# Kernel tuning notes

Measured on AMD Instinct MI355X. Metric: run time of the kernel, lower is better.

## Reference

```python
import jax, jax.numpy as jnp
import numpy as np

N = 60000   # cells
F = 256     # CELL_FEATURE_DIM
H = 128     # HIDDEN_DIM
NH = 8      # NUM_HEADS
DH = H // NH
L = 2       # NUM_LAYERS
C = 256     # tissue clusters
E = 600000  # cell edges
ET = 1500   # tissue edges
NCLS = 4


def _seg_softmax(s, seg, n):
    # numerically stable softmax within segments; s: [E, NH]
    m = jax.ops.segment_max(s, seg, num_segments=n)
    e = jnp.exp(s - m[seg])
    z = jax.ops.segment_sum(e, seg, num_segments=n)
    return e / z[seg]


def _forward(cell_features, cluster_labels, cell_edge_index, tissue_edge_index,
             W_cell_proj, b_cell_proj, W_tissue_proj, b_tissue_proj,
             gat_W, gat_asrc, gat_adst, gat_b, gcn_W, gcn_b,
             bu_Wq, bu_Wk, bu_Wv, bu_bq, bu_bk, bu_bv, bu_Wo, bu_bo,
             td_Wv, td_bv, td_Wo, td_bo,
             gru_Wih, gru_bih, gru_Whh, gru_bhh,
             Wc1, bc1, Wc2, bc2, Wc3, bc3):
    lab = cluster_labels
    # tissue node init = per-cluster mean of raw cell features (as in _construct_tissue_graph)
    cnt = jax.ops.segment_sum(jnp.ones((N,), jnp.float32), lab, num_segments=C)
    tissue_x = jax.ops.segment_sum(cell_features, lab, num_segments=C) / jnp.maximum(cnt, 1.0)[:, None]

    cell_h = cell_features @ W_cell_proj.T + b_cell_proj      # [N, H]
    tissue_h = tissue_x @ W_tissue_proj.T + b_tissue_proj     # [C, H]

    # add self-loops (PyG GATConv / GCNConv default)
    csrc = jnp.concatenate([cell_edge_index[0], jnp.arange(N, dtype=cell_edge_index.dtype)])
    cdst = jnp.concatenate([cell_edge_index[1], jnp.arange(N, dtype=cell_edge_index.dtype)])
    tsrc = jnp.concatenate([tissue_edge_index[0], jnp.arange(C, dtype=tissue_edge_index.dtype)])
    tdst = jnp.concatenate([tissue_edge_index[1], jnp.arange(C, dtype=tissue_edge_index.dtype)])

    # GCN symmetric norm (deg over col, PyG gcn_norm)
    degc = jax.ops.segment_sum(jnp.ones_like(tdst, dtype=jnp.float32), tdst, num_segments=C)
    dinv = jnp.where(degc > 0, 1.0 / jnp.sqrt(degc), 0.0)
    w_e = (dinv[tsrc] * dinv[tdst])[:, None]

    scale = 1.0 / jnp.sqrt(jnp.float32(DH))

    for l in range(L):
        # --- GATConv (multi-head concat) + ELU ---
        h = (cell_h @ gat_W[l].T).reshape(N, NH, DH)
        a_s = (h * gat_asrc[l]).sum(-1)  # [N, NH]
        a_d = (h * gat_adst[l]).sum(-1)
        e = jax.nn.leaky_relu(a_s[csrc] + a_d[cdst], negative_slope=0.2)  # [E+N, NH]
        alpha = _seg_softmax(e, cdst, N)
        agg = jax.ops.segment_sum(h[csrc] * alpha[:, :, None], cdst, num_segments=N)
        cell_h = jax.nn.elu(agg.reshape(N, H) + gat_b[l])

        # --- GCNConv + ReLU on tissue graph ---
        th = tissue_h @ gcn_W[l].T
        tissue_h = jax.nn.relu(jax.ops.segment_sum(th[tsrc] * w_e, tdst, num_segments=C) + gcn_b[l])

        # --- bottom-up cross-level attention: tissue queries attend over their cells ---
        q = ((tissue_h @ bu_Wq.T + bu_bq) * scale).reshape(C, NH, DH)
        k = (cell_h @ bu_Wk.T + bu_bk).reshape(N, NH, DH)
        v = (cell_h @ bu_Wv.T + bu_bv).reshape(N, NH, DH)
        s_att = (q[lab] * k).sum(-1)                       # [N, NH]
        al = _seg_softmax(s_att, lab, C)
        ctx = jax.ops.segment_sum(v * al[:, :, None], lab, num_segments=C).reshape(C, H)
        tissue_h = ctx @ bu_Wo.T + bu_bo

        # --- top-down attention: each cell attends to its single tissue node ---
        # softmax over one key is identically 1, so output = Wo(Wv t + bv) + bo gathered per cell
        td = (tissue_h @ td_Wv.T + td_bv) @ td_Wo.T + td_bo  # [C, H]
        cell_h = td[lab]

        # --- top-down GRUCell refinement: x=[cell;tissue], h=cell ---
        x_in = jnp.concatenate([cell_h, tissue_h[lab]], axis=-1)  # [N, 2H]
        gi = x_in @ gru_Wih.T + gru_bih
        gh = cell_h @ gru_Whh.T + gru_bhh
        r = jax.nn.sigmoid(gi[:, :H] + gh[:, :H])
        z = jax.nn.sigmoid(gi[:, H:2 * H] + gh[:, H:2 * H])
        n = jnp.tanh(gi[:, 2 * H:] + r * gh[:, 2 * H:])
        cell_h = (1.0 - z) * n + z * cell_h

    # dual-pooling readouts (single graph: batch all zeros)
    emb = jnp.concatenate([cell_h.mean(0), cell_h.max(0), tissue_h.mean(0), tissue_h.max(0)])[None, :]  # [1, 4H]
    h1 = jax.nn.relu(emb @ Wc1.T + bc1)
    h2 = jax.nn.relu(h1 @ Wc2.T + bc2)
    return h2 @ Wc3.T + bc3  # [1, NCLS]


def setup_inputs() -> dict:
    k = jax.random.split(jax.random.key(0), 40)
    s = 0.05
    r = lambda i, shape: jax.random.normal(k[i], shape, jnp.float32) * s
    return dict(
        cell_features=jax.random.normal(k[0], (N, F), jnp.float32),
        cell_edge_index=jax.random.randint(k[1], (2, E), 0, N),
        cluster_labels=jax.random.randint(k[2], (N,), 0, C),
        tissue_edge_index=jax.random.randint(k[3], (2, ET), 0, C),
        W_cell_proj=r(4, (H, F)), b_cell_proj=r(5, (H,)),
        W_tissue_proj=r(6, (H, F)), b_tissue_proj=r(7, (H,)),
        gat_W=r(8, (L, H, H)), gat_asrc=r(9, (L, NH, DH)), gat_adst=r(10, (L, NH, DH)), gat_b=r(11, (L, H)),
        gcn_W=r(12, (L, H, H)), gcn_b=r(13, (L, H)),
        bu_Wq=r(14, (H, H)), bu_Wk=r(15, (H, H)), bu_Wv=r(16, (H, H)),
        bu_bq=r(17, (H,)), bu_bk=r(18, (H,)), bu_bv=r(19, (H,)),
        bu_Wo=r(20, (H, H)), bu_bo=r(21, (H,)),
        td_Wv=r(22, (H, H)), td_bv=r(23, (H,)), td_Wo=r(24, (H, H)), td_bo=r(25, (H,)),
        gru_Wih=r(26, (3 * H, 2 * H)), gru_bih=r(27, (3 * H,)),
        gru_Whh=r(28, (3 * H, H)), gru_bhh=r(29, (3 * H,)),
        Wc1=r(30, (2 * H, 4 * H)), bc1=r(31, (2 * H,)),
        Wc2=r(32, (H, 2 * H)), bc2=r(33, (H,)),
        Wc3=r(34, (NCLS, H)), bc3=r(35, (NCLS,)),
    )


def reference(cell_features, cell_edge_index, cluster_labels, tissue_edge_index,
              W_cell_proj, b_cell_proj, W_tissue_proj, b_tissue_proj,
              gat_W, gat_asrc, gat_adst, gat_b, gcn_W, gcn_b,
              bu_Wq, bu_Wk, bu_Wv, bu_bq, bu_bk, bu_bv, bu_Wo, bu_bo,
              td_Wv, td_bv, td_Wo, td_bo,
              gru_Wih, gru_bih, gru_Whh, gru_bhh,
              Wc1, bc1, Wc2, bc2, Wc3, bc3):
    return _forward(cell_features, cluster_labels, cell_edge_index, tissue_edge_index,
                    W_cell_proj, b_cell_proj, W_tissue_proj, b_tissue_proj,
                    gat_W, gat_asrc, gat_adst, gat_b, gcn_W, gcn_b,
                    bu_Wq, bu_Wk, bu_Wv, bu_bq, bu_bk, bu_bv, bu_Wo, bu_bo,
                    td_Wv, td_bv, td_Wo, td_bo,
                    gru_Wih, gru_bih, gru_Whh, gru_bhh,
                    Wc1, bc1, Wc2, bc2, Wc3, bc3)
```

## Files before the change

### kernel.cpp

```cpp
#include <hip/hip_runtime.h>
#include <math.h>

constexpr int N  = 60000;
constexpr int F  = 256;
constexpr int H  = 128;
constexpr int C  = 256;
constexpr int E  = 600000;
constexpr int ET = 1500;
constexpr int NB = (N + 1023) / 1024;
constexpr int SPL = 8;
constexpr int PB  = 16;

typedef __attribute__((ext_vector_type(8))) short short8;
typedef __attribute__((ext_vector_type(4))) float f32x4;

__device__ __forceinline__ unsigned short f2b(float f) {
  unsigned int u = __float_as_uint(f);
  return (unsigned short)((u + 0x7FFFu + ((u >> 16) & 1u)) >> 16);
}
__device__ __forceinline__ float b2f(unsigned short b) {
  return __uint_as_float(((unsigned int)b) << 16);
}

__global__ void hg_hist(const int* __restrict__ cdst, int* __restrict__ deg,
                        const int* __restrict__ lab, int* __restrict__ ccnt) {
  int e = blockIdx.x * 256 + threadIdx.x;
  if (e < E) atomicAdd(&deg[cdst[e]], 1);
  if (e < N) atomicAdd(&ccnt[lab[e]], 1);
}

__global__ __launch_bounds__(256) void hg_scan1(const int* __restrict__ deg, int* __restrict__ off,
                                                int* __restrict__ btot, int n) {
  int b = blockIdx.x, t = threadIdx.x;
  int i0 = b * 1024 + t * 4;
  __shared__ int sums[256];
  int d0 = 0, d1 = 0, d2 = 0, d3 = 0;
  if (i0 + 3 < n) {
    int4 dd = *(const int4*)&deg[i0];
    d0 = dd.x; d1 = dd.y; d2 = dd.z; d3 = dd.w;
  } else {
    if (i0     < n) d0 = deg[i0];
    if (i0 + 1 < n) d1 = deg[i0 + 1];
    if (i0 + 2 < n) d2 = deg[i0 + 2];
    if (i0 + 3 < n) d3 = deg[i0 + 3];
  }
  int s = d0 + d1 + d2 + d3;
  sums[t] = s;
  __syncthreads();
  for (int ofs = 1; ofs < 256; ofs <<= 1) {
    int v = (t >= ofs) ? sums[t - ofs] : 0;
    __syncthreads();
    sums[t] += v;
    __syncthreads();
  }
  int excl = sums[t] - s;
  if (t == 255) btot[b] = sums[t];
  int run = excl;
  if (i0     < n) off[i0]     = run; run += d0;
  if (i0 + 1 < n) off[i0 + 1] = run; run += d1;
  if (i0 + 2 < n) off[i0 + 2] = run; run += d2;
  if (i0 + 3 < n) off[i0 + 3] = run;
}

__global__ __launch_bounds__(256) void hg_scan2_setup(int* __restrict__ btot, int* __restrict__ off,
                                                      const int* __restrict__ ccnt, int* __restrict__ coff,
                                                      const int* __restrict__ tsrc, const int* __restrict__ tdst,
                                                      int* __restrict__ toff, int* __restrict__ tlist,
                                                      float* __restrict__ dinv) {
  __shared__ int sa[256], sb[256], sc2[256];
  int t = threadIdx.x;
  if (blockIdx.x == 0) {
    if (t < 64) sa[t] = (t < NB) ? btot[t] : 0;
    __syncthreads();
    if (t == 0) {
      int r = 0;
      for (int i = 0; i < NB; ++i) { int v = sa[i]; sa[i] = r; r += v; }
      off[N] = r;
    }
    __syncthreads();
    if (t < NB) btot[t] = sa[t];
  } else if (blockIdx.x == 1) {
    int v0 = ccnt[t];
    sa[t] = v0;
    __syncthreads();
    for (int ofs = 1; ofs < 256; ofs <<= 1) {
      int v = (t >= ofs) ? sa[t - ofs] : 0;
      __syncthreads();
      sa[t] += v;
      __syncthreads();
    }
    coff[t + 1] = sa[t];
    if (t == 0) coff[0] = 0;
  } else {
    sa[t] = 0;
    __syncthreads();
    for (int e = t; e < ET; e += 256) atomicAdd(&sa[tdst[e]], 1);
    __syncthreads();
    int v = sa[t];
    dinv[t] = rsqrtf((float)(v + 1));
    sb[t] = v;
    __syncthreads();
    for (int ofs = 1; ofs < 256; ofs <<= 1) {
      int u = (t >= ofs) ? sb[t - ofs] : 0;
      __syncthreads();
      sb[t] += u;
      __syncthreads();
    }
    toff[t + 1] = sb[t];
    if (t == 0) toff[0] = 0;
    sc2[t] = sb[t] - v;
    __syncthreads();
    for (int e = t; e < ET; e += 256) {
      int d = tdst[e];
      int p = atomicAdd(&sc2[d], 1);
      tlist[p] = tsrc[e];
    }
  }
}

__global__ void hg_scan3(int* __restrict__ off, const int* __restrict__ btot, int n) {
  int b = blockIdx.x;
  int addv = btot[b];
  int i0 = b * 1024 + threadIdx.x * 4;
#pragma unroll
  for (int r = 0; r < 4; ++r)
    if (i0 + r < n) off[i0 + r] += addv;
}

__global__ void hg_scatter(const int* __restrict__ csrc, const int* __restrict__ cdst,
                           const int* __restrict__ off, int* __restrict__ cur, int* __restrict__ csr,
                           const int* __restrict__ lab, const int* __restrict__ coff,
                           int* __restrict__ ccur, int* __restrict__ list) {
  int e = blockIdx.x * 256 + threadIdx.x;
  if (e < E) {
    int d = cdst[e];
    int p = atomicAdd(&cur[d], 1);
    csr[off[d] + p] = csrc[e];
  }
  if (e < N) {
    int c = lab[e];
    int p = atomicAdd(&ccur[c], 1);
    list[coff[c] + p] = e;
  }
}

struct TJob { const float* src; float* dst; int SR; int SC; int dld; };
struct PrepArgs {
  TJob j[8];
  const float* gatW1; const float* Wcp; const float* bcp; short* Wcompb; float* bcomp;
  const float* tdWo; const float* tdWv; const float* tdbv; const float* tdbo;
  float* A_td; float* Wcat_t; float* bcat;
  const float* avs; const float* avd; float* sbias;
};

__global__ __launch_bounds__(256) void hg_prep1(PrepArgs a) {
  int y = blockIdx.y, t = threadIdx.x;
  if (y < 8) {
    TJob jb = a.j[y];
    int total = jb.SR * jb.SC;
    for (int idx = blockIdx.x * 256 + t; idx < total; idx += gridDim.x * 256) {
      int r = idx / jb.SC, c = idx - r * jb.SC;
      jb.dst[(size_t)c * jb.dld + r] = jb.src[idx];
    }
  } else if (y == 8) {
    int j = blockIdx.x, k = t;
    float acc = 0.f;
#pragma unroll 4
    for (int m = 0; m < 128; ++m) acc = fmaf(a.gatW1[j * 128 + m], a.Wcp[m * 256 + k], acc);
    a.Wcompb[(size_t)j * 256 + k] = (short)f2b(acc);
    if (k == 0) {
      float b = 0.f;
      for (int m = 0; m < 128; ++m) b = fmaf(a.gatW1[j * 128 + m], a.bcp[m], b);
      a.bcomp[j] = b;
    }
  } else if (y == 9) {
    if (blockIdx.x >= 64) return;
    int j = blockIdx.x * 2 + (t >> 7), k = t & 127;
    float acc = 0.f;
#pragma unroll 4
    for (int p = 0; p < 128; ++p) acc = fmaf(a.tdWo[j * 128 + p], a.tdWv[p * 128 + k], acc);
    a.A_td[j * 128 + k] = acc;
    a.Wcat_t[k * 896 + j] = acc;
    if (k == 0) {
      float b = 0.f;
      for (int p = 0; p < 128; ++p) b = fmaf(a.tdWo[j * 128 + p], a.tdbv[p], b);
      a.bcat[j] = b + a.tdbo[j];
    }
  } else {
    if (blockIdx.x >= 16) return;
    __shared__ float u[128];
    int dir = blockIdx.x >> 3, h = blockIdx.x & 7;
    const float* av = (dir == 0 ? a.avs : a.avd) + h * 16;
    if (t < 128) {
      float s = 0.f;
#pragma unroll
      for (int j = 0; j < 16; ++j) s = fmaf(a.gatW1[(size_t)(h * 16 + j) * 128 + t], av[j], s);
      u[t] = s;
    }
    __syncthreads();
    float q = 0.f;
#pragma unroll 4
    for (int m = 0; m < 128; ++m) q = fmaf(u[m], a.Wcp[m * 256 + t], q);
    a.Wcompb[(size_t)(128 + dir * 8 + h) * 256 + t] = (short)f2b(q);
    if (t == 0) {
      float cs = 0.f;
      for (int m = 0; m < 128; ++m) cs = fmaf(u[m], a.bcp[m], cs);
      a.sbias[dir * 8 + h] = cs;
    }
  }
}

__global__ __launch_bounds__(256) void hg_pc2b(const float* __restrict__ Wih, const float* __restrict__ bih,
                                               const float* __restrict__ Whh, const float* __restrict__ bhh,
                                               const float* __restrict__ A_td, float* __restrict__ Wcat_t,
                                               float* __restrict__ bcat) {
  int jj = blockIdx.x * 2 + (threadIdx.x >> 7), k = threadIdx.x & 127;
  const float* coef;
  float extra, bb;
  int dcol, j;
  if (jj < 384) {
    j = jj; coef = Wih + (size_t)j * 256; extra = Wih[(size_t)j * 256 + 128 + k]; dcol = 128 + j; bb = bih[j];
  } else {
    j = jj - 384; coef = Whh + (size_t)j * 128; extra = 0.f; dcol = 512 + j; bb = bhh[j];
  }
  float a = 0.f;
#pragma unroll 4
  for (int m = 0; m < 128; ++m) a = fmaf(coef[m], A_td[m * 128 + k], a);
  Wcat_t[k * 896 + dcol] = a + extra;
  if (k == 0) {
    float b = 0.f;
    for (int m = 0; m < 128; ++m) b = fmaf(coef[m], bcat[m], b);
    bcat[dcol] = b + bb;
  }
}

__global__ __launch_bounds__(256, 3) void hg_gemm_coef(
    const float* __restrict__ A, int M, int rtiles,
    const short* __restrict__ Wb,
    const float* __restrict__ bias,
    const float* __restrict__ sbias,
    unsigned short* __restrict__ outp,
    float* __restrict__ ab,
    const int* __restrict__ list, const int* __restrict__ coff,
    const float* __restrict__ Wtpt, const float* __restrict__ btp, float* __restrict__ tish) {
  __shared__ float mrow[256];
  const int t = threadIdx.x;

  if (blockIdx.x >= rtiles) {
    int c = blockIdx.x - rtiles;
    int s0 = coff[c], n = coff[c + 1] - s0;
    float acc = 0.f;
#pragma unroll 4
    for (int i = 0; i < n; ++i) acc += A[(size_t)list[s0 + i] * F + t];
    mrow[t] = acc / fmaxf((float)n, 1.f);
    __syncthreads();
    if (t < 128) {
      float a = btp[t];
#pragma unroll 4
      for (int k = 0; k < 256; ++k) a = fmaf(mrow[k], Wtpt[k * 128 + t], a);
      tish[c * 128 + t] = a;
    }
    return;
  }

  const int w = t >> 6, l = t & 63;
  const int li = l & 15, lk = l >> 4;
  const int m0 = blockIdx.x * 128 + w * 32;

  f32x4 zero = {0.f, 0.f, 0.f, 0.f};
  f32x4 acc[2][9];
#pragma unroll
  for (int rt = 0; rt < 2; ++rt)
#pragma unroll
    for (int ct = 0; ct < 9; ++ct) acc[rt][ct] = zero;

  const int r0 = m0 + li, r1 = m0 + 16 + li;
  const bool v0 = r0 < M, v1 = r1 < M;
  const float* a0p = A + (size_t)r0 * 256 + lk * 8;
  const float* a1p = A + (size_t)r1 * 256 + lk * 8;

  for (int kc = 0; kc < 256; kc += 32) {
    short8 bf[9];
#pragma unroll
    for (int ct = 0; ct < 9; ++ct)
      bf[ct] = *(const short8*)&Wb[(size_t)(ct * 16 + li) * 256 + kc + lk * 8];
    short8 af0 = {0, 0, 0, 0, 0, 0, 0, 0};
    short8 af1 = {0, 0, 0, 0, 0, 0, 0, 0};
    if (v0) {
      float4 x = *(const float4*)(a0p + kc);
      float4 y = *(const float4*)(a0p + kc + 4);
      af0[0] = (short)f2b(x.x); af0[1] = (short)f2b(x.y); af0[2] = (short)f2b(x.z); af0[3] = (short)f2b(x.w);
      af0[4] = (short)f2b(y.x); af0[5] = (short)f2b(y.y); af0[6] = (short)f2b(y.z); af0[7] = (short)f2b(y.w);
    }
    if (v1) {
      float4 x = *(const float4*)(a1p + kc);
      float4 y = *(const float4*)(a1p + kc + 4);
      af1[0] = (short)f2b(x.x); af1[1] = (short)f2b(x.y); af1[2] = (short)f2b(x.z); af1[3] = (short)f2b(x.w);
      af1[4] = (short)f2b(y.x); af1[5] = (short)f2b(y.y); af1[6] = (short)f2b(y.z); af1[7] = (short)f2b(y.w);
    }
#pragma unroll
    for (int ct = 0; ct < 9; ++ct) {
      acc[0][ct] = __builtin_amdgcn_mfma_f32_16x16x32_bf16(af0, bf[ct], acc[0][ct], 0, 0, 0);
      acc[1][ct] = __builtin_amdgcn_mfma_f32_16x16x32_bf16(af1, bf[ct], acc[1][ct], 0, 0, 0);
    }
  }

#pragma unroll
  for (int ct = 0; ct < 8; ++ct) {
    float bj = bias[ct * 16 + li];
#pragma unroll
    for (int rt = 0; rt < 2; ++rt) {
#pragma unroll
      for (int r = 0; r < 4; ++r) {
        int gm = m0 + rt * 16 + lk * 4 + r;
        if (gm < M) outp[(size_t)gm * 128 + ct * 16 + li] = f2b(acc[rt][ct][r] + bj);
      }
    }
  }
  {
    float sb = sbias[li];
#pragma unroll
    for (int rt = 0; rt < 2; ++rt) {
#pragma unroll
      for (int r = 0; r < 4; ++r) {
        int gm = m0 + rt * 16 + lk * 4 + r;
        if (gm < M) ab[(size_t)gm * 16 + li] = acc[rt][8][r] + sb;
      }
    }
  }
}

#define GMAXE 64
__global__ __launch_bounds__(256) void hg_gat_agg(
    const unsigned short* __restrict__ hproj, const float* __restrict__ ab,
    const int* __restrict__ off, const int* __restrict__ csr,
    const float* __restrict__ bias, unsigned short* __restrict__ outh,
    const float* __restrict__ qk, const float* __restrict__ qb,
    const int* __restrict__ lab, const int* __restrict__ nodelist,
    float* __restrict__ satt, int nNodes) {
  const int wid = threadIdx.x >> 6;
  const int l = threadIdx.x & 63;
  const int gid = blockIdx.x * 4 + wid;
  __shared__ int srcs_s[4][GMAXE];
  __shared__ float w_s[4][GMAXE][8];
  if (gid >= nNodes) return;
  const int node = nodelist[gid];
  int* srcs = srcs_s[wid];
  float (*wls)[8] = w_s[wid];
  const int o0 = off[node], deg = off[node + 1] - o0;
  const int cl = lab[node];
  const int hsc = l & 7;
  const int q4 = l & 31;
  const int sub = l >> 5;
  const int hq = q4 >> 2;
  const float adh = ab[(size_t)node * 16 + 8 + hsc];
  const float ash = ab[(size_t)node * 16 + hsc];
  float msc = -INFINITY, zsc = 0.f;
  float4 acc = make_float4(0.f, 0.f, 0.f, 0.f);
  const ushort4* hp4 = (const ushort4*)hproj;

  for (int cb = 0; cb < deg; cb += GMAXE) {
    const int len = min(GMAXE, deg - cb);
    if (l < len) srcs[l] = csr[o0 + cb + l];
    asm volatile("s_waitcnt lgkmcnt(0)" ::: "memory");
    float lm = -INFINITY;
    for (int base = 0; base < len; base += 8) {
      int e = base + (l >> 3);
      if (e < len) {
        float sc = ab[(size_t)srcs[e] * 16 + hsc] + adh;
        sc = sc > 0.f ? sc : 0.2f * sc;
        wls[e][hsc] = sc;
        lm = fmaxf(lm, sc);
      }
    }
    lm = fmaxf(lm, __shfl_xor(lm, 8));
    lm = fmaxf(lm, __shfl_xor(lm, 16));
    lm = fmaxf(lm, __shfl_xor(lm, 32));
    float mnew = fmaxf(msc, lm);
    float rs = __expf(msc - mnew);
    float zc = 0.f;
    asm volatile("s_waitcnt lgkmcnt(0)" ::: "memory");
    for (int base = 0; base < len; base += 8) {
      int e = base + (l >> 3);
      if (e < len) {
        float wv = __expf(wls[e][hsc] - mnew);
        wls[e][hsc] = wv;
        zc += wv;
      }
    }
    asm volatile("s_waitcnt lgkmcnt(0)" ::: "memory");
    zc += __shfl_xor(zc, 8); zc += __shfl_xor(zc, 16); zc += __shfl_xor(zc, 32);
    zsc = zsc * rs + zc;
    msc = mnew;
    float rsa = __shfl(rs, hq);
    acc.x *= rsa; acc.y *= rsa; acc.z *= rsa; acc.w *= rsa;
    for (int e = sub; e < len; e += 2) {
      float wv = wls[e][hq];
      ushort4 hv = hp4[(size_t)srcs[e] * 32 + q4];
      acc.x = fmaf(wv, b2f(hv.x), acc.x);
      acc.y = fmaf(wv, b2f(hv.y), acc.y);
      acc.z = fmaf(wv, b2f(hv.z), acc.z);
      acc.w = fmaf(wv, b2f(hv.w), acc.w);
    }
  }
  float ssl = ash + adh;
  ssl = ssl > 0.f ? ssl : 0.2f * ssl;
  float mnew = fmaxf(msc, ssl);
  float rs = __expf(msc - mnew);
  float wsl = __expf(ssl - mnew);
  zsc = zsc * rs + wsl;
  float rsa = __shfl(rs, hq);
  float wsa = __shfl(wsl, hq);
  float zh = __shfl(zsc, hq);
  acc.x *= rsa; acc.y *= rsa; acc.z *= rsa; acc.w *= rsa;
  acc.x += __shfl_xor(acc.x, 32);
  acc.y += __shfl_xor(acc.y, 32);
  acc.z += __shfl_xor(acc.z, 32);
  acc.w += __shfl_xor(acc.w, 32);
  ushort4 hvs = hp4[(size_t)node * 32 + q4];
  acc.x = fmaf(wsa, b2f(hvs.x), acc.x);
  acc.y = fmaf(wsa, b2f(hvs.y), acc.y);
  acc.z = fmaf(wsa, b2f(hvs.z), acc.z);
  acc.w = fmaf(wsa, b2f(hvs.w), acc.w);
  float inv = 1.f / zh;
  float4 bv4 = *(const float4*)&bias[q4 * 4];
  float4 o;
  o.x = acc.x * inv + bv4.x;
  o.y = acc.y * inv + bv4.y;
  o.z = acc.z * inv + bv4.z;
  o.w = acc.w * inv + bv4.w;
  o.x = o.x > 0.f ? o.x : __expf(o.x) - 1.f;
  o.y = o.y > 0.f ? o.y : __expf(o.y) - 1.f;
  o.z = o.z > 0.f ? o.z : __expf(o.z) - 1.f;
  o.w = o.w > 0.f ? o.w : __expf(o.w) - 1.f;
  if (sub == 0) {
    ushort4 ov = make_ushort4(f2b(o.x), f2b(o.y), f2b(o.z), f2b(o.w));
    ((ushort4*)outh)[(size_t)node * 32 + q4] = ov;
  }

  const float4* qk4 = (const float4*)(qk + (size_t)cl * 1024);
  float p0, p1, p2, p3;
  {
    float4 qv0 = qk4[(sub * 4 + 0) * 32 + q4];
    float4 qv1 = qk4[(sub * 4 + 1) * 32 + q4];
    float4 qv2 = qk4[(sub * 4 + 2) * 32 + q4];
    float4 qv3 = qk4[(sub * 4 + 3) * 32 + q4];
    p0 = o.x * qv0.x + o.y * qv0.y + o.z * qv0.z + o.w * qv0.w;
    p1 = o.x * qv1.x + o.y * qv1.y + o.z * qv1.z + o.w * qv1.w;
    p2 = o.x * qv2.x + o.y * qv2.y + o.z * qv2.z + o.w * qv2.w;
    p3 = o.x * qv3.x + o.y * qv3.y + o.z * qv3.z + o.w * qv3.w;
  }
  int b4f = (l >> 4) & 1, b3f = (l >> 3) & 1;
  float snd0 = b4f ? p0 : p2, snd1 = b4f ? p1 : p3;
  float kp0  = b4f ? p2 : p0, kp1  = b4f ? p3 : p1;
  kp0 += __shfl_xor(snd0, 16);
  kp1 += __shfl_xor(snd1, 16);
  float snd = b3f ? kp0 : kp1;
  float kp  = b3f ? kp1 : kp0;
  kp += __shfl_xor(snd, 8);
  kp += __shfl_xor(kp, 4);
  kp += __shfl_xor(kp, 2);
  kp += __shfl_xor(kp, 1);
  int h = sub * 4 + b4f * 2 + b3f;
  if ((l & 7) == 0) satt[(size_t)node * 8 + h] = kp + qb[cl * 8 + h];
}

__global__ __launch_bounds__(256) void hg_ttab(const float* __restrict__ a_sc, const float* __restrict__ a_dc,
                                               float* __restrict__ T) {
  int cd = blockIdx.x, cs = threadIdx.x;
  __shared__ float as[256][8];
  __shared__ float mx[8];
#pragma unroll
  for (int h = 0; h < 8; ++h) as[cs][h] = a_sc[cs * 8 + h];
  __syncthreads();
  if (cs < 8) {
    float m = -INFINITY;
    for (int i = 0; i < 256; ++i) m = fmaxf(m, as[i][cs]);
    mx[cs] = m;
  }
  __syncthreads();
  float* Trow = T + ((size_t)cd * 256 + cs) * 8;
#pragma unroll
  for (int h = 0; h < 8; ++h) {
    float ad = a_dc[cd * 8 + h];
    float s = as[cs][h] + ad;
    s = s > 0.f ? s : 0.2f * s;
    float sm = mx[h] + ad;
    sm = sm > 0.f ? sm : 0.2f * sm;
    Trow[h] = __expf(s - sm);
  }
}

__global__ __launch_bounds__(256) void hg_gat_agg2(
    const unsigned short* __restrict__ hproj,
    const float* __restrict__ T,
    const int* __restrict__ lab, const int* __restrict__ off, const int* __restrict__ csr,
    const float* __restrict__ bias, unsigned short* __restrict__ outh,
    const float* __restrict__ qk, const float* __restrict__ qb,
    const int* __restrict__ nodelist, float* __restrict__ satt, int nNodes) {
  const int wid = threadIdx.x >> 6;
  const int l = threadIdx.x & 63;
  const int gid = blockIdx.x * 4 + wid;
  __shared__ int srcs_s[4][GMAXE];
  if (gid >= nNodes) return;
  const int node = nodelist[gid];
  int* srcs = srcs_s[wid];
  const int o0 = off[node], deg = off[node + 1] - o0;
  const int cd = lab[node];
  const int q4 = l & 31;
  const int sub = l >> 5;
  const int hq = q4 >> 2;
  const float* Trow = T + (size_t)cd * 2048;
  const ushort4* hp4 = (const ushort4*)hproj;
  float4 acc = make_float4(0.f, 0.f, 0.f, 0.f);
  float z = 0.f;

  for (int cb = 0; cb < deg; cb += GMAXE) {
    const int len = min(GMAXE, deg - cb);
    if (l < len) srcs[l] = lab[csr[o0 + cb + l]];
    asm volatile("s_waitcnt lgkmcnt(0)" ::: "memory");
    for (int e = sub; e < len; e += 2) {
      int cs = srcs[e];
      float tw = Trow[cs * 8 + hq];
      ushort4 hv = hp4[(size_t)cs * 32 + q4];
      acc.x = fmaf(tw, b2f(hv.x), acc.x);
      acc.y = fmaf(tw, b2f(hv.y), acc.y);
      acc.z = fmaf(tw, b2f(hv.z), acc.z);
      acc.w = fmaf(tw, b2f(hv.w), acc.w);
      z += tw;
    }
    asm volatile("s_waitcnt lgkmcnt(0)" ::: "memory");
  }
  acc.x += __shfl_xor(acc.x, 32);
  acc.y += __shfl_xor(acc.y, 32);
  acc.z += __shfl_xor(acc.z, 32);
  acc.w += __shfl_xor(acc.w, 32);
  z += __shfl_xor(z, 32);
  {
    float tw = Trow[cd * 8 + hq];
    ushort4 hv = hp4[(size_t)cd * 32 + q4];
    acc.x = fmaf(tw, b2f(hv.x), acc.x);
    acc.y = fmaf(tw, b2f(hv.y), acc.y);
    acc.z = fmaf(tw, b2f(hv.z), acc.z);
    acc.w = fmaf(tw, b2f(hv.w), acc.w);
    z += tw;
  }
  float inv = 1.f / z;
  float4 bv4 = *(const float4*)&bias[q4 * 4];
  float4 o;
  o.x = acc.x * inv + bv4.x;
  o.y = acc.y * inv + bv4.y;
  o.z = acc.z * inv + bv4.z;
  o.w = acc.w * inv + bv4.w;
  o.x = o.x > 0.f ? o.x : __expf(o.x) - 1.f;
  o.y = o.y > 0.f ? o.y : __expf(o.y) - 1.f;
  o.z = o.z > 0.f ? o.z : __expf(o.z) - 1.f;
  o.w = o.w > 0.f ? o.w : __expf(o.w) - 1.f;
  if (sub == 0) {
    ushort4 ov = make_ushort4(f2b(o.x), f2b(o.y), f2b(o.z), f2b(o.w));
    ((ushort4*)outh)[(size_t)node * 32 + q4] = ov;
  }

  const float4* qk4 = (const float4*)(qk + (size_t)cd * 1024);
  float p0, p1, p2, p3;
  {
    float4 qv0 = qk4[(sub * 4 + 0) * 32 + q4];
    float4 qv1 = qk4[(sub * 4 + 1) * 32 + q4];
    float4 qv2 = qk4[(sub * 4 + 2) * 32 + q4];
    float4 qv3 = qk4[(sub * 4 + 3) * 32 + q4];
    p0 = o.x * qv0.x + o.y * qv0.y + o.z * qv0.z + o.w * qv0.w;
    p1 = o.x * qv1.x + o.y * qv1.y + o.z * qv1.z + o.w * qv1.w;
    p2 = o.x * qv2.x + o.y * qv2.y + o.z * qv2.z + o.w * qv2.w;
    p3 = o.x * qv3.x + o.y * qv3.y + o.z * qv3.z + o.w * qv3.w;
  }
  int b4f = (l >> 4) & 1, b3f = (l >> 3) & 1;
  float snd0 = b4f ? p0 : p2, snd1 = b4f ? p1 : p3;
  float kp0  = b4f ? p2 : p0, kp1  = b4f ? p3 : p1;
  kp0 += __shfl_xor(snd0, 16);
  kp1 += __shfl_xor(snd1, 16);
  float snd = b3f ? kp0 : kp1;
  float kp  = b3f ? kp1 : kp0;
  kp += __shfl_xor(snd, 8);
  kp += __shfl_xor(kp, 4);
  kp += __shfl_xor(kp, 2);
  kp += __shfl_xor(kp, 1);
  int h = sub * 4 + b4f * 2 + b3f;
  if ((l & 7) == 0) satt[(size_t)node * 8 + h] = kp + qb[cd * 8 + h];
}

__global__ __launch_bounds__(128) void hg_gcn_q(const float* __restrict__ tin, const int* __restrict__ toff,
                                                const int* __restrict__ tlist, const float* __restrict__ dinv,
                                                const float* __restrict__ gt, const float* __restrict__ gcnb,
                                                const float* __restrict__ Wqt, const float* __restrict__ bq,
                                                const float* __restrict__ Wk, const float* __restrict__ bk,
                                                float* __restrict__ qk, float* __restrict__ qb) {
  int c = blockIdx.x, t = threadIdx.x;
  __shared__ float xa[128], trow[128], qrow[128];
  float dc = dinv[c];
  float acc = tin[c * 128 + t] * dc * dc;
  int s0 = toff[c], s1 = toff[c + 1];
  for (int i = s0; i < s1; ++i) {
    int s = tlist[i];
    acc = fmaf(tin[s * 128 + t], dinv[s] * dc, acc);
  }
  xa[t] = acc;
  __syncthreads();
  float th = 0.f;
#pragma unroll 4
  for (int k = 0; k < 128; ++k) th = fmaf(xa[k], gt[k * 128 + t], th);
  float vv = fmaxf(th + gcnb[t], 0.f);
  trow[t] = vv;
  __syncthreads();
  float qa = bq[t];
#pragma unroll 4
  for (int k = 0; k < 128; ++k) qa = fmaf(trow[k], Wqt[k * 128 + t], qa);
  qrow[t] = qa * 0.25f;
  __syncthreads();
#pragma unroll
  for (int h = 0; h < 8; ++h) {
    float s = 0.f;
#pragma unroll
    for (int j = 0; j < 16; ++j) s = fmaf(Wk[(size_t)(h * 16 + j) * 128 + t], qrow[h * 16 + j], s);
    qk[((size_t)c * 8 + h) * 128 + t] = s;
  }
  if (t < 8) {
    float s = 0.f;
#pragma unroll
    for (int j = 0; j < 16; ++j) s = fmaf(qrow[t * 16 + j], bk[t * 16 + j], s);
    qb[c * 8 + t] = s;
  }
}

__global__ __launch_bounds__(256) void hg_bu_part(
    const float* __restrict__ s_att, const unsigned short* __restrict__ hcell,
    const int* __restrict__ list, const int* __restrict__ coff,
    float* __restrict__ pm, float* __restrict__ pz, float* __restrict__ pmacc) {
  int c = blockIdx.x, sp = blockIdx.y, t = threadIdx.x;
  int s0 = coff[c], n = coff[c + 1] - s0;
  int chunk = (n + SPL - 1) / SPL;
  int b0 = min(n, sp * chunk), b1 = min(n, b0 + chunk);
  int cnt = b1 - b0;
  int tf = t & 127, half = t >> 7;
  __shared__ float red[32][8];
  __shared__ float mh[8];
  __shared__ int cells[64];
  __shared__ float wl[64][8];
  __shared__ float msh[8][128];
  int g = t >> 3, h8 = t & 7;
  float lm = -INFINITY;
  for (int i = g; i < cnt; i += 32) lm = fmaxf(lm, s_att[(size_t)list[s0 + b0 + i] * 8 + h8]);
  red[g][h8] = lm;
  __syncthreads();
  if (t < 8) {
    float m2 = -INFINITY;
#pragma unroll
    for (int i = 0; i < 32; ++i) m2 = fmaxf(m2, red[i][t]);
    mh[t] = m2;
  }
  __syncthreads();
  const float mloc = mh[t & 7];
  float zp = 0.f;
  float macc[8] = {0.f, 0.f, 0.f, 0.f, 0.f, 0.f, 0.f, 0.f};
  for (int cb = 0; cb < cnt; cb += 64) {
    int len = min(64, cnt - cb);
    if (t < len) cells[t] = list[s0 + b0 + cb + t];
    __syncthreads();
#pragma unroll
    for (int p = 0; p < 2; ++p) {
      int e = p * 32 + (t >> 3);
      if (e < len) {
        float w = __expf(s_att[(size_t)cells[e] * 8 + (t & 7)] - mloc);
        wl[e][t & 7] = w;
        zp += w;
      }
    }
    __syncthreads();
    for (int e = half; e < len; e += 2) {
      float x = b2f(hcell[(size_t)cells[e] * 128 + tf]);
      float4 w0 = *(const float4*)&wl[e][0];
      float4 w1 = *(const float4*)&wl[e][4];
      macc[0] = fmaf(w0.x, x, macc[0]);
      macc[1] = fmaf(w0.y, x, macc[1]);
      macc[2] = fmaf(w0.z, x, macc[2]);
      macc[3] = fmaf(w0.w, x, macc[3]);
      macc[4] = fmaf(w1.x, x, macc[4]);
      macc[5] = fmaf(w1.y, x, macc[5]);
      macc[6] = fmaf(w1.z, x, macc[6]);
      macc[7] = fmaf(w1.w, x, macc[7]);
    }
    __syncthreads();
  }
  red[t >> 3][t & 7] = zp;
  __syncthreads();
  int pidx = (c * SPL + sp) * 8;
  if (t < 8) {
    float z = 0.f;
#pragma unroll
    for (int i = 0; i < 32; ++i) z += red[i][t];
    pz[pidx + t] = z;
    pm[pidx + t] = mh[t];
  }
  if (half) {
#pragma unroll
    for (int h = 0; h < 8; ++h) msh[h][tf] = macc[h];
  }
  __syncthreads();
  if (!half) {
#pragma unroll
    for (int h = 0; h < 8; ++h) pmacc[(size_t)(pidx + h) * 128 + tf] = macc[h] + msh[h][tf];
  }
}

__global__ __launch_bounds__(256) void hg_bu_chain(
    const float* __restrict__ pm, const float* __restrict__ pz, const float* __restrict__ pmacc,
    const float* __restrict__ Wv, const float* __restrict__ bv,
    const float* __restrict__ Wot, const float* __restrict__ bo,
    const float* __restrict__ Wcat_t, const float* __restrict__ bcat,
    const float* __restrict__ gatWt, const float* __restrict__ avs, const float* __restrict__ avd,
    float* __restrict__ tish, float* __restrict__ ccell,
    unsigned short* __restrict__ hprojc, float* __restrict__ a_s2, float* __restrict__ a_d2) {
  int c = blockIdx.x, t = threadIdx.x;
  int tf = t & 127, half = t >> 7;
  __shared__ float mh[8], zh[8];
  __shared__ float sscale[SPL][8];
  __shared__ float msh[8][128];
  __shared__ float b0[128], b1[128], part[2][128], catv[896];
  const int pbase = c * SPL * 8;
  if (t < 8) {
    float mg = -INFINITY;
#pragma unroll
    for (int s = 0; s < SPL; ++s) mg = fmaxf(mg, pm[pbase + s * 8 + t]);
    mh[t] = mg;
  }
  __syncthreads();
  if (t < SPL * 8) {
    int s = t >> 3, h = t & 7;
    float ms = pm[pbase + s * 8 + h];
    sscale[s][h] = (ms > -1e37f) ? __expf(ms - mh[h]) : 0.f;
  }
  __syncthreads();
  if (t < 8) {
    float z = 0.f;
#pragma unroll
    for (int s = 0; s < SPL; ++s) z += pz[pbase + s * 8 + t] * sscale[s][t];
    zh[t] = (z > 0.f) ? 1.f / z : 0.f;
  }
  __syncthreads();
#pragma unroll
  for (int hh = 0; hh < 4; ++hh) {
    int h = half * 4 + hh;
    float a = 0.f;
#pragma unroll
    for (int s = 0; s < SPL; ++s)
      a = fmaf(pmacc[(size_t)(pbase + s * 8 + h) * 128 + tf], sscale[s][h], a);
    msh[h][tf] = a * zh[h];
  }
  __syncthreads();
  {
    int h = tf >> 4;
    float ps = 0.f;
    const float* wp = Wv + (size_t)tf * 128 + half * 64;
    const float* mp = &msh[h][half * 64];
#pragma unroll 4
    for (int k = 0; k < 64; ++k) ps = fmaf(wp[k], mp[k], ps);
    part[half][tf] = ps;
  }
  __syncthreads();
  if (t < 128) b0[t] = part[0][t] + part[1][t] + bv[t];
  __syncthreads();
  int ks = half;
  {
    float ps = 0.f;
    const float* wp = Wot + (size_t)ks * 64 * 128 + tf;
#pragma unroll 4
    for (int k = 0; k < 64; ++k) ps = fmaf(b0[ks * 64 + k], wp[k * 128], ps);
    part[ks][tf] = ps;
  }
  __syncthreads();
  if (t < 128) {
    float vv = part[0][t] + part[1][t] + bo[t];
    b1[t] = vv;
    tish[c * 128 + t] = vv;
  }
  __syncthreads();
  for (int j = t; j < 896; j += 256) {
    float a = bcat[j];
#pragma unroll 4
    for (int k = 0; k < 128; ++k) a = fmaf(b1[k], Wcat_t[k * 896 + j], a);
    catv[j] = a;
  }
  __syncthreads();
  if (t < 128) {
    float td = catv[t];
    float r = 1.f / (1.f + expf(-(catv[128 + t] + catv[512 + t])));
    float zz = 1.f / (1.f + expf(-(catv[256 + t] + catv[640 + t])));
    float nn = tanhf(catv[384 + t] + r * catv[768 + t]);
    float cn = (1.f - zz) * nn + zz * td;
    ccell[c * 128 + t] = cn;
    b0[t] = cn;
  }
  __syncthreads();
  if (gatWt) {
    float ps = 0.f;
    const float* wp = gatWt + (size_t)ks * 64 * 128 + tf;
#pragma unroll 4
    for (int k = 0; k < 64; ++k) ps = fmaf(b0[ks * 64 + k], wp[k * 128], ps);
    part[ks][tf] = ps;
    __syncthreads();
    if (t < 128) {
      float hp = part[0][t] + part[1][t];
      hprojc[c * 128 + t] = f2b(hp);
      float pss = hp * avs[t], pdd = hp * avd[t];
      pss += __shfl_xor(pss, 1); pss += __shfl_xor(pss, 2); pss += __shfl_xor(pss, 4); pss += __shfl_xor(pss, 8);
      pdd += __shfl_xor(pdd, 1); pdd += __shfl_xor(pdd, 2); pdd += __shfl_xor(pdd, 4); pdd += __shfl_xor(pdd, 8);
      if ((t & 15) == 0) {
        a_s2[c * 8 + (t >> 4)] = pss;
        a_d2[c * 8 + (t >> 4)] = pdd;
      }
    }
  }
}

__global__ __launch_bounds__(256) void hg_pool(const float* __restrict__ ccell2, const float* __restrict__ tish,
                                               const int* __restrict__ cnt, float* __restrict__ part) {
  int b = blockIdx.x, t = threadIdx.x;
  int c0 = b * (C / PB);
  if (t < 128) {
    float sm = 0.f, mx = -INFINITY;
#pragma unroll 4
    for (int i = 0; i < C / PB; ++i) {
      int c = c0 + i;
      float vv = ccell2[c * 128 + t];
      int n = cnt[c];
      sm += (float)n * vv;
      if (n > 0) mx = fmaxf(mx, vv);
    }
    part[b * 512 + t] = sm;
    part[b * 512 + 128 + t] = mx;
  } else {
    int tt = t - 128;
    float sm = 0.f, mx = -INFINITY;
#pragma unroll 4
    for (int i = 0; i < C / PB; ++i) {
      int c = c0 + i;
      float vv = tish[c * 128 + tt];
      sm += vv;
      mx = fmaxf(mx, vv);
    }
    part[b * 512 + 256 + tt] = sm;
    part[b * 512 + 384 + tt] = mx;
  }
}

__global__ __launch_bounds__(256) void hg_mlp(const float* __restrict__ part, const float* __restrict__ Wc1t,
                                              const float* __restrict__ bc1, const float* __restrict__ Wc2t,
                                              const float* __restrict__ bc2, const float* __restrict__ Wc3,
                                              const float* __restrict__ bc3, float* __restrict__ outp) {
  __shared__ float emb[512], h1s[256], h2s[128];
  int t = threadIdx.x;
  if (t < 128) {
    float sm = 0.f, mx = -INFINITY;
#pragma unroll
    for (int b = 0; b < PB; ++b) {
      sm += part[b * 512 + t];
      mx = fmaxf(mx, part[b * 512 + 128 + t]);
    }
    emb[t] = sm / (float)N;
    emb[128 + t] = mx;
  } else {
    int tt = t - 128;
    float sm = 0.f, mx = -INFINITY;
#pragma unroll
    for (int b = 0; b < PB; ++b) {
      sm += part[b * 512 + 256 + tt];
      mx = fmaxf(mx, part[b * 512 + 384 + tt]);
    }
    emb[256 + tt] = sm * (1.f / (float)C);
    emb[384 + tt] = mx;
  }
  __syncthreads();
  float a = bc1[t];
#pragma unroll 4
  for (int kk = 0; kk < 512; ++kk) a = fmaf(emb[kk], Wc1t[kk * 256 + t], a);
  h1s[t] = fmaxf(a, 0.f);
  __syncthreads();
  if (t < 128) {
    float a2 = bc2[t];
#pragma unroll 4
    for (int kk = 0; kk < 256; ++kk) a2 = fmaf(h1s[kk], Wc2t[kk * 128 + t], a2);
    h2s[t] = fmaxf(a2, 0.f);
  }
  __syncthreads();
  if (t < 4) {
    float o = bc3[t];
    for (int kk = 0; kk < 128; ++kk) o = fmaf(h2s[kk], Wc3[t * 128 + kk], o);
    outp[t] = o;
  }
}

extern "C" void kernel_launch(void* const* d_in, const int* in_sizes, int n_in,
                              void* d_out, int out_size, void* d_ws, size_t ws_size,
                              hipStream_t stream) {
  (void)in_sizes; (void)n_in; (void)out_size; (void)ws_size;
  const float* feat  = (const float*)d_in[0];
  const int*   eidx  = (const int*)d_in[1];
  const int*   lab   = (const int*)d_in[2];
  const int*   tidx  = (const int*)d_in[3];
  const float* Wcp   = (const float*)d_in[4];
  const float* bcp   = (const float*)d_in[5];
  const float* Wtp   = (const float*)d_in[6];
  const float* btp   = (const float*)d_in[7];
  const float* gatW  = (const float*)d_in[8];
  const float* gasrc = (const float*)d_in[9];
  const float* gadst = (const float*)d_in[10];
  const float* gatb  = (const float*)d_in[11];
  const float* gcnW  = (const float*)d_in[12];
  const float* gcnb  = (const float*)d_in[13];
  const float* buWq  = (const float*)d_in[14];
  const float* buWk  = (const float*)d_in[15];
  const float* buWv  = (const float*)d_in[16];
  const float* bubq  = (const float*)d_in[17];
  const float* bubk  = (const float*)d_in[18];
  const float* bubv  = (const float*)d_in[19];
  const float* buWo  = (const float*)d_in[20];
  const float* bubo  = (const float*)d_in[21];
  const float* tdWv  = (const float*)d_in[22];
  const float* tdbv  = (const float*)d_in[23];
  const float* tdWo  = (const float*)d_in[24];
  const float* tdbo  = (const float*)d_in[25];
  const float* Wih   = (const float*)d_in[26];
  const float* bih   = (const float*)d_in[27];
  const float* Whh   = (const float*)d_in[28];
  const float* bhh   = (const float*)d_in[29];
  const float* Wc1   = (const float*)d_in[30];
  const float* bc1   = (const float*)d_in[31];
  const float* Wc2   = (const float*)d_in[32];
  const float* bc2   = (const float*)d_in[33];
  const float* Wc3   = (const float*)d_in[34];
  const float* bc3   = (const float*)d_in[35];
  float* outp = (float*)d_out;

  const int* csrc = eidx;
  const int* cdst = eidx + E;
  const int* tsrc = tidx;
  const int* tdst = tidx + ET;

  char* w = (char*)d_ws;
  auto alloc = [&](size_t bytes) -> void* {
    void* p = (void*)w;
    w += (bytes + 255) & ~(size_t)255;
    return p;
  };
  char* cnt0 = w;
  int* deg_cell = (int*)alloc((size_t)N * 4);
  int* cur_cell = (int*)alloc((size_t)N * 4);
  int* clu_cnt  = (int*)alloc((size_t)C * 4);
  int* clu_cur  = (int*)alloc((size_t)C * 4);
  size_t cntBytes = (size_t)(w - cnt0);
  int* off_cell = (int*)alloc((size_t)(N + 1) * 4);
  int* btot     = (int*)alloc(64 * 4);
  int* csr      = (int*)alloc((size_t)E * 4);
  int* clu_off  = (int*)alloc((size_t)(C + 1) * 4);
  int* clu_list = (int*)alloc((size_t)N * 4);
  int* toff     = (int*)alloc((size_t)(C + 1) * 4);
  int* tlist    = (int*)alloc((size_t)ET * 4);
  float* dinv   = (float*)alloc((size_t)C * 4);
  unsigned short* buf1 = (unsigned short*)alloc((size_t)N * 128 * 2);
  unsigned short* buf2 = (unsigned short*)alloc((size_t)N * 128 * 2);
  float* ab     = (float*)alloc((size_t)N * 16 * 4);
  float* s_att  = (float*)alloc((size_t)N * 8 * 4);
  float* tish   = (float*)alloc((size_t)C * 128 * 4);
  float* qkb    = (float*)alloc((size_t)C * 8 * 128 * 4);
  float* qbb    = (float*)alloc((size_t)C * 8 * 4);
  float* ccell  = (float*)alloc((size_t)C * 128 * 4);
  unsigned short* hprojc = (unsigned short*)alloc((size_t)C * 128 * 2);
  float* a_sc   = (float*)alloc((size_t)C * 8 * 4);
  float* a_dc   = (float*)alloc((size_t)C * 8 * 4);
  float* Ttab   = (float*)alloc((size_t)C * 256 * 8 * 4);
  float* pm     = (float*)alloc((size_t)C * SPL * 8 * 4);
  float* pz     = (float*)alloc((size_t)C * SPL * 8 * 4);
  float* pmacc  = (float*)alloc((size_t)C * SPL * 8 * 128 * 4);
  float* poolp  = (float*)alloc((size_t)PB * 512 * 4);
  float* A_td   = (float*)alloc(128 * 128 * 4);
  float* Wcat_t = (float*)alloc(128 * 896 * 4);
  float* bcat   = (float*)alloc(896 * 4);
  short* Wcompb = (short*)alloc(144 * 256 * 2);
  float* bcomp  = (float*)alloc(128 * 4);
  float* sbias  = (float*)alloc(16 * 4);
  float* Wtpt   = (float*)alloc(256 * 128 * 4);
  float* g1t    = (float*)alloc(128 * 128 * 4);
  float* g2t    = (float*)alloc(128 * 128 * 4);
  float* Wqt    = (float*)alloc(128 * 128 * 4);
  float* Wot    = (float*)alloc(128 * 128 * 4);
  float* gatW2t = (float*)alloc(128 * 128 * 4);
  float* Wc1t   = (float*)alloc(512 * 256 * 4);
  float* Wc2t   = (float*)alloc(256 * 128 * 4);

  hipMemsetAsync(cnt0, 0, cntBytes, stream);

  hg_hist<<<(E + 255) / 256, 256, 0, stream>>>(cdst, deg_cell, lab, clu_cnt);
  hg_scan1<<<NB, 256, 0, stream>>>(deg_cell, off_cell, btot, N);
  hg_scan2_setup<<<3, 256, 0, stream>>>(btot, off_cell, clu_cnt, clu_off, tsrc, tdst, toff, tlist, dinv);
  hg_scan3<<<NB, 256, 0, stream>>>(off_cell, btot, N);
  hg_scatter<<<(E + 255) / 256, 256, 0, stream>>>(csrc, cdst, off_cell, cur_cell, csr,
                                                  lab, clu_off, clu_cur, clu_list);

  PrepArgs pa;
  pa.j[0] = {Wtp,            Wtpt,   128, 256, 128};
  pa.j[1] = {gcnW,           g1t,    128, 128, 128};
  pa.j[2] = {gcnW + 128*128, g2t,    128, 128, 128};
  pa.j[3] = {buWq,           Wqt,    128, 128, 128};
  pa.j[4] = {buWo,           Wot,    128, 128, 128};
  pa.j[5] = {gatW + 128*128, gatW2t, 128, 128, 128};
  pa.j[6] = {Wc1,            Wc1t,   256, 512, 256};
  pa.j[7] = {Wc2,            Wc2t,   128, 256, 128};
  pa.gatW1 = gatW; pa.Wcp = Wcp; pa.bcp = bcp; pa.Wcompb = Wcompb; pa.bcomp = bcomp;
  pa.tdWo = tdWo; pa.tdWv = tdWv; pa.tdbv = tdbv; pa.tdbo = tdbo;
  pa.A_td = A_td; pa.Wcat_t = Wcat_t; pa.bcat = bcat;
  pa.avs = gasrc; pa.avd = gadst; pa.sbias = sbias;
  hg_prep1<<<dim3(128, 11), 256, 0, stream>>>(pa);
  hg_pc2b<<<384, 256, 0, stream>>>(Wih, bih, Whh, bhh, A_td, Wcat_t, bcat);

  const int RT = (N + 127) / 128;
  hg_gemm_coef<<<RT + C, 256, 0, stream>>>(feat, N, RT, Wcompb, bcomp, sbias, buf2, ab,
                                           clu_list, clu_off, Wtpt, btp, tish);
  hg_gcn_q<<<C, 128, 0, stream>>>(tish, toff, tlist, dinv, g1t, gcnb, Wqt, bubq, buWk, bubk, qkb, qbb);
  hg_gat_agg<<<(N + 3) / 4, 256, 0, stream>>>(buf2, ab, off_cell, csr, gatb, buf1,
                                              qkb, qbb, lab, clu_list, s_att, N);
  hg_bu_part<<<dim3(C, SPL), 256, 0, stream>>>(s_att, buf1, clu_list, clu_off, pm, pz, pmacc);
  hg_bu_chain<<<C, 256, 0, stream>>>(pm, pz, pmacc, buWv, bubv, Wot, bubo, Wcat_t, bcat,
                                     gatW2t, gasrc + 128, gadst + 128, tish, ccell, hprojc, a_sc, a_dc);
  hg_gcn_q<<<C, 128, 0, stream>>>(tish, toff, tlist, dinv, g2t, gcnb + 128, Wqt, bubq, buWk, bubk, qkb, qbb);
  hg_ttab<<<C, 256, 0, stream>>>(a_sc, a_dc, Ttab);
  hg_gat_agg2<<<(N + 3) / 4, 256, 0, stream>>>(hprojc, Ttab, lab, off_cell, csr, gatb + 128, buf1,
                                               qkb, qbb, clu_list, s_att, N);
  hg_bu_part<<<dim3(C, SPL), 256, 0, stream>>>(s_att, buf1, clu_list, clu_off, pm, pz, pmacc);
  hg_bu_chain<<<C, 256, 0, stream>>>(pm, pz, pmacc, buWv, bubv, Wot, bubo, Wcat_t, bcat,
                                     nullptr, nullptr, nullptr, tish, ccell, nullptr, nullptr, nullptr);

  hg_pool<<<PB, 256, 0, stream>>>(ccell, tish, clu_cnt, poolp);
  hg_mlp<<<1, 256, 0, stream>>>(poolp, Wc1t, bc1, Wc2t, bc2, Wc3, bc3, outp);
}
```

Baseline: 557.4 us.

## Shrink coef GEMM tile to 64 rows, prefetch A, split attention-score outputs

The projection GEMM now gives each wave 16 rows instead of 32, which halves the accumulators, raises the occupancy hint from 3 to 4, and doubles the grid. The next k-chunk of A is loaded before the current chunk is converted and multiplied, so the global load latency overlaps the MFMA work. The per-node source and destination attention scores are written to two separate [N,8] arrays instead of one interleaved [N,16] array, which makes the per-edge source-score gathers in the GAT aggregation denser. In exchange, every B-fragment load of the weights is now amortised over half as many rows, so weight traffic per row doubles.

```diff
diff --git a/kernel.cpp b/kernel.cpp
--- a/kernel.cpp
+++ b/kernel.cpp
@@ -234,13 +234,13 @@
   }
 }
 
-__global__ __launch_bounds__(256, 3) void hg_gemm_coef(
+__global__ __launch_bounds__(256, 4) void hg_gemm_coef(
     const float* __restrict__ A, int M, int rtiles,
     const short* __restrict__ Wb,
     const float* __restrict__ bias,
     const float* __restrict__ sbias,
     unsigned short* __restrict__ outp,
-    float* __restrict__ ab,
+    float* __restrict__ o_s, float* __restrict__ o_d,
     const int* __restrict__ list, const int* __restrict__ coff,
     const float* __restrict__ Wtpt, const float* __restrict__ btp, float* __restrict__ tish) {
   __shared__ float mrow[256];
@@ -265,66 +265,60 @@
 
   const int w = t >> 6, l = t & 63;
   const int li = l & 15, lk = l >> 4;
-  const int m0 = blockIdx.x * 128 + w * 32;
+  const int rbase = blockIdx.x * 64 + w * 16;
+  const int row = rbase + li;
+  const bool v = row < M;
+  const float* ap = A + (size_t)row * 256 + lk * 8;
 
   f32x4 zero = {0.f, 0.f, 0.f, 0.f};
-  f32x4 acc[2][9];
-#pragma unroll
-  for (int rt = 0; rt < 2; ++rt)
-#pragma unroll
-    for (int ct = 0; ct < 9; ++ct) acc[rt][ct] = zero;
-
-  const int r0 = m0 + li, r1 = m0 + 16 + li;
-  const bool v0 = r0 < M, v1 = r1 < M;
-  const float* a0p = A + (size_t)r0 * 256 + lk * 8;
-  const float* a1p = A + (size_t)r1 * 256 + lk * 8;
-
+  f32x4 acc[9];
+#pragma unroll
+  for (int ct = 0; ct < 9; ++ct) acc[ct] = zero;
+
+  float4 x, y;
+  if (v) {
+    x = *(const float4*)ap;
+    y = *(const float4*)(ap + 4);
+  }
   for (int kc = 0; kc < 256; kc += 32) {
+    float4 nx, ny;
+    if (v && kc + 32 < 256) {
+      nx = *(const float4*)(ap + kc + 32);
+      ny = *(const float4*)(ap + kc + 36);
+    }
     short8 bf[9];
 #pragma unroll
     for (int ct = 0; ct < 9; ++ct)
       bf[ct] = *(const short8*)&Wb[(size_t)(ct * 16 + li) * 256 + kc + lk * 8];
-    short8 af0 = {0, 0, 0, 0, 0, 0, 0, 0};
-    short8 af1 = {0, 0, 0, 0, 0, 0, 0, 0};
-    if (v0) {
-      float4 x = *(const float4*)(a0p + kc);
-      float4 y = *(const float4*)(a0p + kc + 4);
-      af0[0] = (short)f2b(x.x); af0[1] = (short)f2b(x.y); af0[2] = (short)f2b(x.z); af0[3] = (short)f2b(x.w);
-      af0[4] = (short)f2b(y.x); af0[5] = (short)f2b(y.y); af0[6] = (short)f2b(y.z); af0[7] = (short)f2b(y.w);
-    }
-    if (v1) {
-      float4 x = *(const float4*)(a1p + kc);
-      float4 y = *(const float4*)(a1p + kc + 4);
-      af1[0] = (short)f2b(x.x); af1[1] = (short)f2b(x.y); af1[2] = (short)f2b(x.z); af1[3] = (short)f2b(x.w);
-      af1[4] = (short)f2b(y.x); af1[5] = (short)f2b(y.y); af1[6] = (short)f2b(y.z); af1[7] = (short)f2b(y.w);
-    }
-#pragma unroll
-    for (int ct = 0; ct < 9; ++ct) {
-      acc[0][ct] = __builtin_amdgcn_mfma_f32_16x16x32_bf16(af0, bf[ct], acc[0][ct], 0, 0, 0);
-      acc[1][ct] = __builtin_amdgcn_mfma_f32_16x16x32_bf16(af1, bf[ct], acc[1][ct], 0, 0, 0);
-    }
+    short8 af = {0, 0, 0, 0, 0, 0, 0, 0};
+    if (v) {
+      af[0] = (short)f2b(x.x); af[1] = (short)f2b(x.y); af[2] = (short)f2b(x.z); af[3] = (short)f2b(x.w);
+      af[4] = (short)f2b(y.x); af[5] = (short)f2b(y.y); af[6] = (short)f2b(y.z); af[7] = (short)f2b(y.w);
+    }
+#pragma unroll
+    for (int ct = 0; ct < 9; ++ct)
+      acc[ct] = __builtin_amdgcn_mfma_f32_16x16x32_bf16(af, bf[ct], acc[ct], 0, 0, 0);
+    x = nx; y = ny;
   }
 
 #pragma unroll
   for (int ct = 0; ct < 8; ++ct) {
     float bj = bias[ct * 16 + li];
 #pragma unroll
-    for (int rt = 0; rt < 2; ++rt) {
-#pragma unroll
-      for (int r = 0; r < 4; ++r) {
-        int gm = m0 + rt * 16 + lk * 4 + r;
-        if (gm < M) outp[(size_t)gm * 128 + ct * 16 + li] = f2b(acc[rt][ct][r] + bj);
-      }
+    for (int r = 0; r < 4; ++r) {
+      int gm = rbase + lk * 4 + r;
+      if (gm < M) outp[(size_t)gm * 128 + ct * 16 + li] = f2b(acc[ct][r] + bj);
     }
   }
   {
     float sb = sbias[li];
 #pragma unroll
-    for (int rt = 0; rt < 2; ++rt) {
-#pragma unroll
-      for (int r = 0; r < 4; ++r) {
-        int gm = m0 + rt * 16 + lk * 4 + r;
-        if (gm < M) ab[(size_t)gm * 16 + li] = acc[rt][8][r] + sb;
+    for (int r = 0; r < 4; ++r) {
+      int gm = rbase + lk * 4 + r;
+      if (gm < M) {
+        float vv = acc[8][r] + sb;
+        if (li < 8) o_s[(size_t)gm * 8 + li] = vv;
+        else        o_d[(size_t)gm * 8 + (li - 8)] = vv;
       }
     }
   }
@@ -332,7 +326,8 @@
 
 #define GMAXE 64
 __global__ __launch_bounds__(256) void hg_gat_agg(
-    const unsigned short* __restrict__ hproj, const float* __restrict__ ab,
+    const unsigned short* __restrict__ hproj, const float* __restrict__ a_s,
+    const float* __restrict__ a_d,
     const int* __restrict__ off, const int* __restrict__ csr,
     const float* __restrict__ bias, unsigned short* __restrict__ outh,
     const float* __restrict__ qk, const float* __restrict__ qb,
@@ -353,8 +348,8 @@
   const int q4 = l & 31;
   const int sub = l >> 5;
   const int hq = q4 >> 2;
-  const float adh = ab[(size_t)node * 16 + 8 + hsc];
-  const float ash = ab[(size_t)node * 16 + hsc];
+  const float adh = a_d[(size_t)node * 8 + hsc];
+  const float ash = a_s[(size_t)node * 8 + hsc];
   float msc = -INFINITY, zsc = 0.f;
   float4 acc = make_float4(0.f, 0.f, 0.f, 0.f);
   const ushort4* hp4 = (const ushort4*)hproj;
@@ -367,7 +362,7 @@
     for (int base = 0; base < len; base += 8) {
       int e = base + (l >> 3);
       if (e < len) {
-        float sc = ab[(size_t)srcs[e] * 16 + hsc] + adh;
+        float sc = a_s[(size_t)srcs[e] * 8 + hsc] + adh;
         sc = sc > 0.f ? sc : 0.2f * sc;
         wls[e][hsc] = sc;
         lm = fmaxf(lm, sc);
@@ -967,7 +962,8 @@
   float* dinv   = (float*)alloc((size_t)C * 4);
   unsigned short* buf1 = (unsigned short*)alloc((size_t)N * 128 * 2);
   unsigned short* buf2 = (unsigned short*)alloc((size_t)N * 128 * 2);
-  float* ab     = (float*)alloc((size_t)N * 16 * 4);
+  float* a_s    = (float*)alloc((size_t)N * 8 * 4);
+  float* a_d    = (float*)alloc((size_t)N * 8 * 4);
   float* s_att  = (float*)alloc((size_t)N * 8 * 4);
   float* tish   = (float*)alloc((size_t)C * 128 * 4);
   float* qkb    = (float*)alloc((size_t)C * 8 * 128 * 4);
@@ -1021,11 +1017,11 @@
   hg_prep1<<<dim3(128, 11), 256, 0, stream>>>(pa);
   hg_pc2b<<<384, 256, 0, stream>>>(Wih, bih, Whh, bhh, A_td, Wcat_t, bcat);
 
-  const int RT = (N + 127) / 128;
-  hg_gemm_coef<<<RT + C, 256, 0, stream>>>(feat, N, RT, Wcompb, bcomp, sbias, buf2, ab,
+  const int RT = (N + 63) / 64;
+  hg_gemm_coef<<<RT + C, 256, 0, stream>>>(feat, N, RT, Wcompb, bcomp, sbias, buf2, a_s, a_d,
                                            clu_list, clu_off, Wtpt, btp, tish);
   hg_gcn_q<<<C, 128, 0, stream>>>(tish, toff, tlist, dinv, g1t, gcnb, Wqt, bubq, buWk, bubk, qkb, qbb);
-  hg_gat_agg<<<(N + 3) / 4, 256, 0, stream>>>(buf2, ab, off_cell, csr, gatb, buf1,
+  hg_gat_agg<<<(N + 3) / 4, 256, 0, stream>>>(buf2, a_s, a_d, off_cell, csr, gatb, buf1,
                                               qkb, qbb, lab, clu_list, s_att, N);
   hg_bu_part<<<dim3(C, SPL), 256, 0, stream>>>(s_att, buf1, clu_list, clu_off, pm, pz, pmacc);
   hg_bu_chain<<<C, 256, 0, stream>>>(pm, pz, pmacc, buWv, bubv, Wot, bubo, Wcat_t, bcat,
```

Result: slower. 578.7 us (+3.8%).
